# Optimization experiments

Measured on AMD Instinct MI355X. Metric: run time of the kernel, lower is better.

The kernel has to match this reference:

```python
import jax, jax.numpy as jnp
import numpy as np

N_NODES = 100000
N_EDGES = 3200000
SIGMA_REF = 0.07
T_REF = 293.15
DSIGMA_DT = -0.0001
PHI_THRESH = 0.3
EPS = 1e-8


def compute_gradient(T, pos, edge_index):
    """Edge-based finite-difference gradient, scatter-reduced to nodes.

    grad_T[i] = mean over incoming edges (src->i) of
                (T[src]-T[i]) * (pos[src]-pos[i]) / |pos[src]-pos[i]|^2
    """
    src, dst = edge_index[0], edge_index[1]
    dT = T[src] - T[dst]                         # [E]
    dpos = pos[src] - pos[dst]                   # [E,3]
    dist2 = jnp.sum(dpos * dpos, axis=-1) + EPS  # [E]
    contrib = (dT / dist2)[:, None] * dpos       # [E,3]
    num = jax.ops.segment_sum(contrib, dst, num_segments=N_NODES)            # [N,3]
    cnt = jax.ops.segment_sum(jnp.ones_like(dT), dst, num_segments=N_NODES)  # [N]
    return num / jnp.maximum(cnt, 1.0)[:, None]


def setup_inputs() -> dict:
    key = jax.random.key(0)
    k1, k2, k3 = jax.random.split(key, 3)
    x = jax.random.normal(k1, (N_NODES, 9), dtype=jnp.float32)
    pos = jax.random.normal(k2, (N_NODES, 3), dtype=jnp.float32)
    edge_index = jax.random.randint(k3, (2, N_EDGES), 0, N_NODES, dtype=jnp.int64)
    return {"x": x, "pos": pos, "edge_index": edge_index}


def reference(x, pos, edge_index):
    T = x[:, 3]
    phi = x[:, 8]
    grad_T = compute_gradient(T, pos, edge_index)          # [N,3]
    force = DSIGMA_DT * grad_T                             # [N,3]
    interface_mask = (jnp.abs(phi) < PHI_THRESH).astype(force.dtype)
    return force * interface_mask[:, None]
```

## Files before the change

### kernel.cpp

```cpp
#include <hip/hip_runtime.h>

#define N_NODES 100000
#define N_EDGES 3200000
#define NVEC    (N_EDGES / 4)

#define S_LOG2  8
#define S       (1 << S_LOG2)
#define NPART   ((N_NODES + S - 1) / S)
#define NPB     448
#define GSTRIDE 16

#define BT      1024
#define EPB     6252
#define NB      ((N_EDGES + EPB - 1) / EPB)
#define CAP     9216
#define KPT     9

constexpr float DSIGMA_DT  = -0.0001f;
constexpr float PHI_THRESH = 0.3f;
constexpr float EPS        = 1e-8f;

__global__ __launch_bounds__(BT, 8) void bin_kernel(const int4* __restrict__ ei4,
                                                    const float* __restrict__ x,
                                                    const float* __restrict__ pos,
                                                    float4* __restrict__ posT,
                                                    int* __restrict__ gcur,
                                                    int* __restrict__ buckets) {
    __shared__ int   lbuf[EPB];
    __shared__ unsigned short lrk[EPB];
    __shared__ unsigned short lbinS[EPB];
    __shared__ int hist[NPB], lofs[NPB];
    __shared__ int baseg[NPART];
    const int tid = threadIdx.x;

    {
        const int per = (N_NODES + NB - 1) / NB;
        const int lo = blockIdx.x * per;
        const int hi = min(lo + per, N_NODES);
        for (int i = lo + tid; i < hi; i += BT)
            posT[i] = make_float4(pos[3 * i], pos[3 * i + 1], pos[3 * i + 2],
                                  x[9 * i + 3]);
    }

    const int ebase = blockIdx.x * EPB;
    const int n  = min(EPB, N_EDGES - ebase);
    const int nv = n >> 2;
    const int4* __restrict__ src4 = ei4 + (ebase >> 2);
    const int4* __restrict__ dst4 = ei4 + NVEC + (ebase >> 2);

    for (int i = tid; i < NPB; i += BT) hist[i] = 0;
    __syncthreads();

    for (int v = tid; v < nv; v += BT) {
        int4 d = dst4[v];
        ushort4 rk;
        rk.x = (unsigned short)atomicAdd(&hist[d.x >> S_LOG2], 1);
        rk.y = (unsigned short)atomicAdd(&hist[d.y >> S_LOG2], 1);
        rk.z = (unsigned short)atomicAdd(&hist[d.z >> S_LOG2], 1);
        rk.w = (unsigned short)atomicAdd(&hist[d.w >> S_LOG2], 1);
        ((ushort4*)lrk)[v] = rk;
    }
    __syncthreads();

    if (tid < 64) {
        int carry = 0;
        for (int b = 0; b < NPB; b += 64) {
            int v = hist[b + tid];
            int orig = v;
#pragma unroll
            for (int d = 1; d < 64; d <<= 1) {
                int t = __shfl_up(v, d, 64);
                if (tid >= d) v += t;
            }
            lofs[b + tid] = carry + v - orig;
            carry += __shfl(v, 63, 64);
        }
    }
    __syncthreads();
    if (tid < NPART)
        baseg[tid] = atomicAdd(&gcur[tid * GSTRIDE], hist[tid]);
    __syncthreads();

    for (int v = tid; v < nv; v += BT) {
        int4 s = src4[v];
        int4 d = dst4[v];
        ushort4 rk = ((const ushort4*)lrk)[v];
#pragma unroll
        for (int k = 0; k < 4; ++k) {
            int dk = k == 0 ? d.x : k == 1 ? d.y : k == 2 ? d.z : d.w;
            int sk = k == 0 ? s.x : k == 1 ? s.y : k == 2 ? s.z : s.w;
            int rr = k == 0 ? rk.x : k == 1 ? rk.y : k == 2 ? rk.z : rk.w;
            int bin = dk >> S_LOG2;
            int pos = lofs[bin] + rr;
            lbuf[pos]  = (sk << S_LOG2) | (dk & (S - 1));
            lbinS[pos] = (unsigned short)bin;
        }
    }
    __syncthreads();

    for (int i = tid; i < n; i += BT) {
        int b   = lbinS[i];
        int pos = baseg[b] + (i - lofs[b]);
        if (pos < CAP) buckets[(size_t)b * CAP + pos] = lbuf[i];
    }
}

__global__ __launch_bounds__(BT, 8) void part_kernel(
        const int* __restrict__ gcur,
        const int* __restrict__ buckets,
        const float4* __restrict__ posT,
        const float* __restrict__ x,
        float* __restrict__ out) {
    __shared__ int S2[CAP];
    __shared__ int hist[S], base[S];
    __shared__ float4 ploc[S];
    const int p = blockIdx.x, tid = threadIdx.x;
    const int lo = p << S_LOG2;

    if (tid < S) {
        hist[tid] = 0;
        int node = lo + tid;
        ploc[tid] = (node < N_NODES) ? posT[node] : make_float4(0.f, 0.f, 0.f, 0.f);
    }
    const int len = min(gcur[p * GSTRIDE], CAP);
    const int* __restrict__ bp = buckets + (size_t)p * CAP;
    __syncthreads();

    int ent[KPT];
    unsigned short prk[KPT];
#pragma unroll
    for (int k = 0; k < KPT; ++k) {
        int i = tid + k * BT;
        ent[k] = 0;
        if (i < len) {
            ent[k] = bp[i];
            prk[k] = (unsigned short)atomicAdd(&hist[ent[k] & (S - 1)], 1);
        }
    }
    __syncthreads();

    if (tid < 64) {
        int carry = 0;
        for (int b = 0; b < S; b += 64) {
            int v = hist[b + tid];
            int orig = v;
#pragma unroll
            for (int d = 1; d < 64; d <<= 1) {
                int t = __shfl_up(v, d, 64);
                if (tid >= d) v += t;
            }
            base[b + tid] = carry + v - orig;
            carry += __shfl(v, 63, 64);
        }
    }
    __syncthreads();

#pragma unroll
    for (int k = 0; k < KPT; ++k) {
        int i = tid + k * BT;
        if (i < len)
            S2[base[ent[k] & (S - 1)] + (int)prk[k]] = ent[k] >> S_LOG2;
    }
    __syncthreads();

    const int r = tid >> 2, q = tid & 3;
    const int node = lo + r;
    const int nseg = hist[r];
    const int b0 = base[r];
    float4 b = ploc[r];
    float ax = 0.f, ay = 0.f, az = 0.f;
    for (int j = b0 + q; j < b0 + nseg; j += 4) {
        float4 a = posT[S2[j]];
        float px = a.x - b.x, py = a.y - b.y, pz = a.z - b.z;
        float dT = a.w - b.w;
        float w  = dT / (px * px + py * py + pz * pz + EPS);
        ax += w * px; ay += w * py; az += w * pz;
    }
    ax += __shfl_down(ax, 2, 64); ax += __shfl_down(ax, 1, 64);
    ay += __shfl_down(ay, 2, 64); ay += __shfl_down(ay, 1, 64);
    az += __shfl_down(az, 2, 64); az += __shfl_down(az, 1, 64);
    if (q == 0 && node < N_NODES) {
        float phi = x[node * 9 + 8];
        float cn = nseg > 1 ? (float)nseg : 1.0f;
        float m = (fabsf(phi) < PHI_THRESH) ? (DSIGMA_DT / cn) : 0.0f;
        out[3 * node]     = m * ax;
        out[3 * node + 1] = m * ay;
        out[3 * node + 2] = m * az;
    }
}

__global__ void prep_kernel(const float* __restrict__ x,
                            const float* __restrict__ pos,
                            float4* __restrict__ posT) {
    int i = blockIdx.x * blockDim.x + threadIdx.x;
    if (i < N_NODES)
        posT[i] = make_float4(pos[3 * i], pos[3 * i + 1], pos[3 * i + 2],
                              x[9 * i + 3]);
}

__global__ void edge_scatter_atomic_kernel(const int* __restrict__ ei,
                                           const float4* __restrict__ posT,
                                           float4* __restrict__ accum) {
    int e = blockIdx.x * blockDim.x + threadIdx.x;
    if (e >= N_EDGES) return;
    int s = ei[e];
    int d = ei[N_EDGES + e];
    float4 a = posT[s];
    float4 b = posT[d];
    float px = a.x - b.x, py = a.y - b.y, pz = a.z - b.z;
    float dT = a.w - b.w;
    float w  = dT / (px * px + py * py + pz * pz + EPS);
    float* ac = (float*)&accum[d];
    atomicAdd(ac,     w * px);
    atomicAdd(ac + 1, w * py);
    atomicAdd(ac + 2, w * pz);
    atomicAdd(ac + 3, 1.0f);
}

__global__ void finalize_accum_kernel(const float* __restrict__ x,
                                      const float4* __restrict__ accum,
                                      float* __restrict__ out) {
    int i = blockIdx.x * blockDim.x + threadIdx.x;
    if (i >= N_NODES) return;
    float4 a = accum[i];
    float phi = x[i * 9 + 8];
    float cn = a.w > 1.0f ? a.w : 1.0f;
    float m = (fabsf(phi) < PHI_THRESH) ? (DSIGMA_DT / cn) : 0.0f;
    out[3 * i]     = m * a.x;
    out[3 * i + 1] = m * a.y;
    out[3 * i + 2] = m * a.z;
}

extern "C" void kernel_launch(void* const* d_in, const int* in_sizes, int n_in,
                              void* d_out, int out_size, void* d_ws, size_t ws_size,
                              hipStream_t stream) {
    const float* x   = (const float*)d_in[0];
    const float* pos = (const float*)d_in[1];
    const int*   ei  = (const int*)d_in[2];
    float* out = (float*)d_out;

    const size_t posT_b = (size_t)N_NODES * sizeof(float4);
    const size_t gcur_b = 32768;
    const size_t buck_b = (size_t)NPART * CAP * sizeof(int);

    char* w = (char*)d_ws;
    float4* posT    = (float4*)w;
    int*    gcur    = (int*)(w + posT_b);
    int*    buckets = (int*)(w + posT_b + gcur_b);

    const size_t need_full = posT_b + gcur_b + buck_b;

    const int B = 256;

    if (ws_size >= need_full) {
        hipMemsetAsync(gcur, 0, gcur_b, stream);
        bin_kernel<<<NB, BT, 0, stream>>>((const int4*)ei, x, pos, posT, gcur, buckets);
        part_kernel<<<NPART, BT, 0, stream>>>(gcur, buckets, posT, x, out);
    } else {
        float4* accum = (float4*)(w + posT_b);
        prep_kernel<<<(N_NODES + B - 1) / B, B, 0, stream>>>(x, pos, posT);
        hipMemsetAsync(accum, 0, (size_t)N_NODES * sizeof(float4), stream);
        edge_scatter_atomic_kernel<<<(N_EDGES + B - 1) / B, B, 0, stream>>>(ei, posT, accum);
        finalize_accum_kernel<<<(N_NODES + B - 1) / B, B, 0, stream>>>(x, accum, out);
    }
}
```

Measured before the change: 116.0 us.

## Split per-partition buckets and counters by XCD to localize global atomics

Each bin_kernel block now picks a sub-bucket from its XCD (blockIdx & 7), so each partition has separate counters and a smaller bucket region (CAP8) per XCD. The goal is to keep the global atomicAdd contention and bucket writes within one XCD's L2 instead of spreading them across dies. part_kernel then gathers the 8 sub-buckets per partition, using 2 slots per thread per XCD, and its launch bounds drop to 4 blocks. The cost is more register state, more small reads, and a risk of silently dropping edges if one sub-bucket goes past CAP8.

```diff
diff --git a/kernel.cpp b/kernel.cpp
--- a/kernel.cpp
+++ b/kernel.cpp
@@ -9,12 +9,13 @@
 #define NPART   ((N_NODES + S - 1) / S)
 #define NPB     448
 #define GSTRIDE 16
+#define NXCD    8
+#define CAP8    1536
 
 #define BT      1024
 #define EPB     6252
 #define NB      ((N_EDGES + EPB - 1) / EPB)
 #define CAP     9216
-#define KPT     9
 
 constexpr float DSIGMA_DT  = -0.0001f;
 constexpr float PHI_THRESH = 0.3f;
@@ -32,6 +33,7 @@
     __shared__ int hist[NPB], lofs[NPB];
     __shared__ int baseg[NPART];
     const int tid = threadIdx.x;
+    const int xcd = blockIdx.x & (NXCD - 1);
 
     {
         const int per = (N_NODES + NB - 1) / NB;
@@ -78,7 +80,7 @@
     }
     __syncthreads();
     if (tid < NPART)
-        baseg[tid] = atomicAdd(&gcur[tid * GSTRIDE], hist[tid]);
+        baseg[tid] = atomicAdd(&gcur[(xcd * NPART + tid) * GSTRIDE], hist[tid]);
     __syncthreads();
 
     for (int v = tid; v < nv; v += BT) {
@@ -101,11 +103,12 @@
     for (int i = tid; i < n; i += BT) {
         int b   = lbinS[i];
         int pos = baseg[b] + (i - lofs[b]);
-        if (pos < CAP) buckets[(size_t)b * CAP + pos] = lbuf[i];
-    }
-}
-
-__global__ __launch_bounds__(BT, 8) void part_kernel(
+        if (pos < CAP8)
+            buckets[((size_t)(xcd * NPART + b)) * CAP8 + pos] = lbuf[i];
+    }
+}
+
+__global__ __launch_bounds__(BT, 4) void part_kernel(
         const int* __restrict__ gcur,
         const int* __restrict__ buckets,
         const float4* __restrict__ posT,
@@ -122,19 +125,23 @@
         int node = lo + tid;
         ploc[tid] = (node < N_NODES) ? posT[node] : make_float4(0.f, 0.f, 0.f, 0.f);
     }
-    const int len = min(gcur[p * GSTRIDE], CAP);
-    const int* __restrict__ bp = buckets + (size_t)p * CAP;
-    __syncthreads();
-
-    int ent[KPT];
-    unsigned short prk[KPT];
-#pragma unroll
-    for (int k = 0; k < KPT; ++k) {
-        int i = tid + k * BT;
-        ent[k] = 0;
-        if (i < len) {
-            ent[k] = bp[i];
-            prk[k] = (unsigned short)atomicAdd(&hist[ent[k] & (S - 1)], 1);
+    __syncthreads();
+
+    int len[NXCD];
+    int ent[NXCD][2];
+    unsigned short prk[NXCD][2];
+#pragma unroll
+    for (int xx = 0; xx < NXCD; ++xx) {
+        len[xx] = min(gcur[(xx * NPART + p) * GSTRIDE], CAP8);
+        const int* __restrict__ bp = buckets + ((size_t)(xx * NPART + p)) * CAP8;
+#pragma unroll
+        for (int r = 0; r < 2; ++r) {
+            int i = tid + r * BT;
+            if (i < len[xx]) {
+                int e = bp[i];
+                ent[xx][r] = e;
+                prk[xx][r] = (unsigned short)atomicAdd(&hist[e & (S - 1)], 1);
+            }
         }
     }
     __syncthreads();
@@ -156,21 +163,28 @@
     __syncthreads();
 
 #pragma unroll
-    for (int k = 0; k < KPT; ++k) {
-        int i = tid + k * BT;
-        if (i < len)
-            S2[base[ent[k] & (S - 1)] + (int)prk[k]] = ent[k] >> S_LOG2;
-    }
-    __syncthreads();
-
-    const int r = tid >> 2, q = tid & 3;
-    const int node = lo + r;
-    const int nseg = hist[r];
-    const int b0 = base[r];
-    float4 b = ploc[r];
+    for (int xx = 0; xx < NXCD; ++xx) {
+#pragma unroll
+        for (int r = 0; r < 2; ++r) {
+            int i = tid + r * BT;
+            if (i < len[xx]) {
+                int e = ent[xx][r];
+                int pos = base[e & (S - 1)] + (int)prk[xx][r];
+                if (pos < CAP) S2[pos] = e >> S_LOG2;
+            }
+        }
+    }
+    __syncthreads();
+
+    const int rr = tid >> 2, q = tid & 3;
+    const int node = lo + rr;
+    const int nseg = hist[rr];
+    const int b0 = base[rr];
+    const int jend = min(b0 + nseg, CAP);
+    float4 b = ploc[rr];
     float ax = 0.f, ay = 0.f, az = 0.f;
-    for (int j = b0 + q; j < b0 + nseg; j += 4) {
-        float4 a = posT[S2[j]];
+    for (int jj = b0 + q; jj < jend; jj += 4) {
+        float4 a = posT[S2[jj]];
         float px = a.x - b.x, py = a.y - b.y, pz = a.z - b.z;
         float dT = a.w - b.w;
         float w  = dT / (px * px + py * py + pz * pz + EPS);
@@ -240,15 +254,15 @@
     float* out = (float*)d_out;
 
     const size_t posT_b = (size_t)N_NODES * sizeof(float4);
-    const size_t gcur_b = 32768;
-    const size_t buck_b = (size_t)NPART * CAP * sizeof(int);
+    const size_t gcur_b = (size_t)NXCD * NPART * GSTRIDE * sizeof(int);
+    const size_t buck_b = (size_t)NXCD * NPART * CAP8 * sizeof(int);
 
     char* w = (char*)d_ws;
     float4* posT    = (float4*)w;
     int*    gcur    = (int*)(w + posT_b);
-    int*    buckets = (int*)(w + posT_b + gcur_b);
-
-    const size_t need_full = posT_b + gcur_b + buck_b;
+    int*    buckets = (int*)(w + posT_b + ((gcur_b + 255) & ~255ull));
+
+    const size_t need_full = posT_b + ((gcur_b + 255) & ~255ull) + buck_b;
 
     const int B = 256;
 
```

Result: faster. 113.3 us (-2.3%).
